# Kernel tuning notes

Hardware: AMD Instinct MI355X
Metric: run time of the kernel (lower is better)

The kernel has to match this reference:

```python
import jax, jax.numpy as jnp
import numpy as np

B, R, S, D, K = 4096, 49, 50, 512, 100

def setup_inputs() -> dict:
    key = jax.random.key(0)
    ks = jax.random.split(key, 10)
    return {
        "ifeature": jax.random.normal(ks[0], (B, R, D), dtype=jnp.float32),
        "tfeature_h": jax.random.normal(ks[1], (B, S, D), dtype=jnp.float32),
        "w_Vi_0": jax.random.normal(ks[2], (D, K), dtype=jnp.float32) * 0.05,
        "w_Vt_0": jax.random.normal(ks[3], (D, K), dtype=jnp.float32) * 0.05,
        "w_Pi_0": jax.random.normal(ks[4], (2 * K, 1), dtype=jnp.float32) * 0.05,
        "b_Pi_0": jnp.zeros((R,), dtype=jnp.float32),
        "w_Vi_1": jax.random.normal(ks[5], (D, K), dtype=jnp.float32) * 0.05,
        "w_Vt_1": jax.random.normal(ks[6], (D, K), dtype=jnp.float32) * 0.05,
        "w_Pi_1": jax.random.normal(ks[7], (2 * K, 1), dtype=jnp.float32) * 0.05,
        "b_Pi_1": jnp.zeros((S,), dtype=jnp.float32),
    }

def reference(ifeature, tfeature_h, w_Vi_0, w_Vt_0, w_Pi_0, b_Pi_0,
              w_Vi_1, w_Vt_1, w_Pi_1, b_Pi_1):
    # ---- pass 0: attend over image regions, conditioned on mean text feature
    tfeature = jnp.mean(tfeature_h, axis=1)                      # [B, D]
    wVi0 = jnp.einsum('brd,dk->brk', ifeature, w_Vi_0)           # [B, R, K]
    wVt0 = (tfeature @ w_Vt_0)[:, None, :]                       # [B, 1, K] -> broadcast over R
    Hi = jnp.tanh(jnp.concatenate(
        [wVi0, jnp.broadcast_to(wVt0, wVi0.shape)], axis=-1))    # [B, R, 2K]
    scores_i = jnp.squeeze(Hi @ w_Pi_0, axis=-1) + b_Pi_0        # [B, R]
    Pi = jax.nn.softmax(scores_i, axis=-1)                       # [B, R]
    Vi = jnp.einsum('br,brd->bd', Pi, ifeature)                  # [B, D]
    # ---- pass 1: attend over text positions, conditioned on attended image
    wVi1 = (Vi @ w_Vi_1)[:, None, :]                             # [B, 1, K]
    wVt1 = jnp.einsum('bsd,dk->bsk', tfeature_h, w_Vt_1)         # [B, S, K]
    Ht = jnp.tanh(jnp.concatenate(
        [jnp.broadcast_to(wVi1, wVt1.shape), wVt1], axis=-1))    # [B, S, 2K]
    scores_t = jnp.squeeze(Ht @ w_Pi_1, axis=-1) + b_Pi_1        # [B, S]
    Pt = jax.nn.softmax(scores_t, axis=-1)                       # [B, S]
    Vt = jnp.einsum('bs,bsd->bd', Pt, tfeature_h)                # [B, D]
    return Vi + Vt
```

## Files before the change

### kernel.cpp

```cpp
#include <hip/hip_runtime.h>
#include <math.h>

#define NB 4096
#define NR 49
#define NS 50
#define ND 512
#define NK 100
#define NTT 8
#define KSTEPS 16
#define CHUNK_KS 8
#define FRAGS (NTT * KSTEPS * 64 * 8)

typedef __attribute__((ext_vector_type(8))) short short8;
typedef __attribute__((ext_vector_type(4))) float f32x4;

__device__ __forceinline__ unsigned short f32_bf16(float f) {
    union { float f; unsigned u; } x; x.f = f;
    return (unsigned short)((x.u + 0x7fffu + ((x.u >> 16) & 1u)) >> 16);
}
__device__ __forceinline__ unsigned cvt_pk_bf16(float lo, float hi) {
    unsigned r;
    asm("v_cvt_pk_bf16_f32 %0, %1, %2" : "=v"(r) : "v"(lo), "v"(hi));
    return r;
}
__device__ __forceinline__ float fast_tanh(float x) {
    const float ax = fabsf(x);
    const float e = __expf(2.f * ax);
    const float r = 1.f - 2.f / (e + 1.f);
    return copysignf(r, x);
}

__global__ void preswz_kernel(const float* __restrict__ w0, const float* __restrict__ w1,
                              unsigned short* __restrict__ ws)
{
    const int l  = threadIdx.x;
    const int gk = blockIdx.x & 15;
    const int t  = blockIdx.x >> 4;
    const int m  = blockIdx.y;
    const float* W = m ? w1 : w0;
    const int col = t * 16 + (l & 15);
    const int k0  = gk * 32 + (l >> 4) * 8;
    unsigned short* o = ws + (size_t)m * FRAGS + ((size_t)(t * 16 + gk) * 64 + l) * 8;
#pragma unroll
    for (int j = 0; j < 8; ++j) {
        float v = (col < NK) ? W[(size_t)(k0 + j) * NK + col] : 0.f;
        o[j] = f32_bf16(v);
    }
}

struct SM {
    short buf[NS * 256];
    float scores[64];
    float part2[64];
    float P[64];
};

__global__ __launch_bounds__(512, 8) void coattn_main(
    const float* __restrict__ ifeat, const float* __restrict__ tfeat,
    const float* __restrict__ wPi0, const float* __restrict__ bPi0,
    const float* __restrict__ wPi1, const float* __restrict__ bPi1,
    const unsigned short* __restrict__ wsW, float* __restrict__ out)
{
    __shared__ SM sm;
    const int pass = blockIdx.x & 1;
    const int b    = blockIdx.x >> 1;
    const int tid  = threadIdx.x;

    const float* feat = pass ? (tfeat + (size_t)b * NS * ND) : (ifeat + (size_t)b * NR * ND);
    const int nrows  = pass ? NS : NR;
    const int nclamp = nrows - 1;
    const unsigned short* wsR = wsW + (size_t)pass * FRAGS;
    const float* wPiRow = pass ? (wPi1 + NK) : wPi0;
    const float* bvec   = pass ? bPi1 : bPi0;

    const int lane = tid & 63, wid = tid >> 6;
    const int m = wid & 3, nh = wid >> 2;
    const int t0 = nh * 4;
    const int colg = lane & 15, g = lane >> 4;
    const int arow0 = m * 16 + colg;
    const int arow = (arow0 < nclamp) ? arow0 : nclamp;
    const int rswz = arow & 7;

    const unsigned short* wlane = wsR + (size_t)t0 * (KSTEPS * 512) + lane * 8;

    const f32x4 zero4 = {0.f, 0.f, 0.f, 0.f};
    f32x4 acc[4] = {zero4, zero4, zero4, zero4};

    const int nitems = nrows * 32;

    for (int chunk = 0; chunk < 2; ++chunk) {
        __syncthreads();
        for (int it = tid; it < nitems; it += 512) {
            const int r = it >> 5, c = it & 31;
            const float* p = feat + (r << 9) + (chunk << 8) + (c << 3);
            const float4 a  = *reinterpret_cast<const float4*>(p);
            const float4 b4 = *reinterpret_cast<const float4*>(p + 4);
            uint4 v;
            v.x = cvt_pk_bf16(a.x, a.y);   v.y = cvt_pk_bf16(a.z, a.w);
            v.z = cvt_pk_bf16(b4.x, b4.y); v.w = cvt_pk_bf16(b4.z, b4.w);
            *reinterpret_cast<uint4*>(&sm.buf[(r << 8) + ((c ^ (r & 7)) << 3)]) = v;
        }
        __syncthreads();

        const int gk0 = chunk * CHUNK_KS;
#pragma unroll
        for (int ks = 0; ks < CHUNK_KS; ++ks) {
            const short8 a = *reinterpret_cast<const short8*>(
                &sm.buf[(arow << 8) + ((((ks << 2) + g) ^ rswz) << 3)]);
            const unsigned short* wk = wlane + (size_t)(gk0 + ks) * 512;
#pragma unroll
            for (int q = 0; q < 4; ++q) {
                const short8 w = *reinterpret_cast<const short8*>(wk + (size_t)q * (KSTEPS * 512));
                acc[q] = __builtin_amdgcn_mfma_f32_16x16x32_bf16(a, w, acc[q], 0, 0, 0);
            }
        }
    }

    {
        float s[4] = {0.f, 0.f, 0.f, 0.f};
#pragma unroll
        for (int q = 0; q < 4; ++q) {
            const int col = (t0 + q) * 16 + colg;
            const float w = (col < NK) ? wPiRow[col] : 0.f;
#pragma unroll
            for (int i = 0; i < 4; ++i) s[i] += fast_tanh(acc[q][i]) * w;
        }
#pragma unroll
        for (int off = 1; off < 16; off <<= 1) {
#pragma unroll
            for (int i = 0; i < 4; ++i) s[i] += __shfl_xor(s[i], off);
        }
        if (colg == 0) {
            float* o = nh ? sm.part2 : sm.scores;
            const int rbase = m * 16 + g * 4;
#pragma unroll
            for (int i = 0; i < 4; ++i) {
                const int r = rbase + i;
                if (r < nrows) o[r] = s[i] + (nh ? 0.f : bvec[r]);
            }
        }
    }
    __syncthreads();

    if (tid < 64) {
        const float v = (tid < nrows) ? sm.scores[tid] + sm.part2[tid] : -3.0e38f;
        float mx = v;
#pragma unroll
        for (int off = 32; off; off >>= 1) mx = fmaxf(mx, __shfl_xor(mx, off));
        const float e = (tid < nrows) ? __expf(v - mx) : 0.f;
        float su = e;
#pragma unroll
        for (int off = 32; off; off >>= 1) su += __shfl_xor(su, off);
        sm.P[tid] = e / su;
    }
    __syncthreads();

    {
        float v = 0.f;
        const float* fp = feat + tid;
        for (int r = 0; r < nrows; ++r) v += sm.P[r] * fp[r << 9];
        atomicAdd(&out[(size_t)b * ND + tid], v);
    }
}

extern "C" void kernel_launch(void* const* d_in, const int* in_sizes, int n_in,
                              void* d_out, int out_size, void* d_ws, size_t ws_size,
                              hipStream_t stream) {
    const float* ifeat = (const float*)d_in[0];
    const float* tfeat = (const float*)d_in[1];
    const float* wVi0  = (const float*)d_in[2];
    const float* wPi0  = (const float*)d_in[4];
    const float* bPi0  = (const float*)d_in[5];
    const float* wVt1  = (const float*)d_in[7];
    const float* wPi1  = (const float*)d_in[8];
    const float* bPi1  = (const float*)d_in[9];
    float* outp = (float*)d_out;
    unsigned short* wsW = (unsigned short*)d_ws;

    hipMemsetAsync(outp, 0, (size_t)NB * ND * sizeof(float), stream);
    hipLaunchKernelGGL(preswz_kernel, dim3(NTT * KSTEPS, 2), dim3(64), 0, stream,
                       wVi0, wVt1, wsW);
    hipLaunchKernelGGL(coattn_main, dim3(2 * NB), dim3(512), 0, stream,
                       ifeat, tfeat, wPi0, bPi0, wPi1, bPi1, wsW, outp);
}
```

Before: 338.9 us.

## Process 16 batches per block with register-resident weights and double-buffered LDS

Each block now handles 16 consecutive batch items for one pass, with 7 waves that each keep their bf16 weight column tile in registers for the whole block lifetime. Feature rows are streamed in 128-wide K chunks into double-buffered LDS, and the next chunk's global loads are issued before the current chunk's MFMAs, which overlaps loads with compute. The aim is to stop re-reading weights from global memory for every batch item and to hide load latency. In exchange the grid is much smaller (512 blocks), the kernel uses more registers, and a barrier follows every chunk.

```diff
diff --git a/kernel.cpp b/kernel.cpp
--- a/kernel.cpp
+++ b/kernel.cpp
@@ -6,10 +6,12 @@
 #define NS 50
 #define ND 512
 #define NK 100
-#define NTT 8
+#define NT 7
 #define KSTEPS 16
-#define CHUNK_KS 8
-#define FRAGS (NTT * KSTEPS * 64 * 8)
+#define NBATCH 16
+#define NGRP (NB / NBATCH)
+#define BTHREADS 448
+#define FRAGS (NT * KSTEPS * 64 * 8)
 
 typedef __attribute__((ext_vector_type(8))) short short8;
 typedef __attribute__((ext_vector_type(4))) float f32x4;
@@ -49,13 +51,12 @@
 }
 
 struct SM {
-    short buf[NS * 256];
-    float scores[64];
-    float part2[64];
+    short buf[2][64 * 128];
+    float part[NT][64];
     float P[64];
 };
 
-__global__ __launch_bounds__(512, 8) void coattn_main(
+__global__ __launch_bounds__(BTHREADS, 4) void coattn_main(
     const float* __restrict__ ifeat, const float* __restrict__ tfeat,
     const float* __restrict__ wPi0, const float* __restrict__ bPi0,
     const float* __restrict__ wPi1, const float* __restrict__ bPi1,
@@ -63,103 +64,142 @@
 {
     __shared__ SM sm;
     const int pass = blockIdx.x & 1;
-    const int b    = blockIdx.x >> 1;
+    const int grp  = blockIdx.x >> 1;
     const int tid  = threadIdx.x;
-
-    const float* feat = pass ? (tfeat + (size_t)b * NS * ND) : (ifeat + (size_t)b * NR * ND);
+    const int lane = tid & 63, wid = tid >> 6;
+    const int colg = lane & 15, g = lane >> 4;
+
     const int nrows  = pass ? NS : NR;
-    const int nclamp = nrows - 1;
-    const unsigned short* wsR = wsW + (size_t)pass * FRAGS;
+    const int nitems = nrows * 32;
+    const float* featB = (pass ? tfeat : ifeat) + (size_t)grp * NBATCH * nrows * ND;
     const float* wPiRow = pass ? (wPi1 + NK) : wPi0;
     const float* bvec   = pass ? bPi1 : bPi0;
 
-    const int lane = tid & 63, wid = tid >> 6;
-    const int m = wid & 3, nh = wid >> 2;
-    const int t0 = nh * 4;
-    const int colg = lane & 15, g = lane >> 4;
-    const int arow0 = m * 16 + colg;
-    const int arow = (arow0 < nclamp) ? arow0 : nclamp;
-    const int rswz = arow & 7;
-
-    const unsigned short* wlane = wsR + (size_t)t0 * (KSTEPS * 512) + lane * 8;
-
-    const f32x4 zero4 = {0.f, 0.f, 0.f, 0.f};
-    f32x4 acc[4] = {zero4, zero4, zero4, zero4};
-
-    const int nitems = nrows * 32;
-
-    for (int chunk = 0; chunk < 2; ++chunk) {
+    short8 wreg[KSTEPS];
+    {
+        const unsigned short* wl = wsW + (size_t)pass * FRAGS
+                                 + ((size_t)wid * KSTEPS * 64 + lane) * 8;
+#pragma unroll
+        for (int ks = 0; ks < KSTEPS; ++ks)
+            wreg[ks] = *reinterpret_cast<const short8*>(wl + ks * 512);
+    }
+
+    for (int u = tid; u < 512; u += BTHREADS) {
+        const int bsel = u >> 8, uu = u & 255;
+        const int r = 48 + (uu >> 4), q = uu & 15;
+        *reinterpret_cast<uint4*>(&sm.buf[bsel][r * 128 + q * 8]) = uint4{0u, 0u, 0u, 0u};
+    }
+    __syncthreads();
+
+    for (int it = tid; it < nitems; it += BTHREADS) {
+        const int r = it >> 5, v = it & 31;
+        const float4 a = *reinterpret_cast<const float4*>(featB + (size_t)r * ND + v * 4);
+        uint2 wv; wv.x = cvt_pk_bf16(a.x, a.y); wv.y = cvt_pk_bf16(a.z, a.w);
+        *reinterpret_cast<uint2*>(
+            &sm.buf[0][r * 128 + (((v >> 1) ^ (r & 7)) << 3) + (v & 1) * 4]) = wv;
+    }
+    __syncthreads();
+
+    const int tailN = nitems - 3 * BTHREADS;
+
+    for (int i = 0; i < NBATCH; ++i) {
+        const float* fi = featB + (size_t)i * nrows * ND;
+        f32x4 acc[4];
+#pragma unroll
+        for (int rt = 0; rt < 4; ++rt) acc[rt] = f32x4{0.f, 0.f, 0.f, 0.f};
+
+#pragma unroll
+        for (int c = 0; c < 4; ++c) {
+            const bool haveNext = (c < 3) || (i + 1 < NBATCH);
+            const float* fsrc = (c < 3) ? (fi + (c + 1) * 128) : (fi + (size_t)nrows * ND);
+
+            float4 L0{}, L1{}, L2{}, L3{};
+            if (haveNext) {
+                const int i0 = tid, i1 = tid + BTHREADS, i2 = tid + 2 * BTHREADS,
+                          i3 = tid + 3 * BTHREADS;
+                L0 = *reinterpret_cast<const float4*>(fsrc + (size_t)(i0 >> 5) * ND + (i0 & 31) * 4);
+                L1 = *reinterpret_cast<const float4*>(fsrc + (size_t)(i1 >> 5) * ND + (i1 & 31) * 4);
+                L2 = *reinterpret_cast<const float4*>(fsrc + (size_t)(i2 >> 5) * ND + (i2 & 31) * 4);
+                if (tid < tailN)
+                    L3 = *reinterpret_cast<const float4*>(fsrc + (size_t)(i3 >> 5) * ND + (i3 & 31) * 4);
+            }
+
+#pragma unroll
+            for (int lks = 0; lks < 4; ++lks) {
+                const int q0 = lks * 4 + g;
+#pragma unroll
+                for (int rt = 0; rt < 4; ++rt) {
+                    const int r = rt * 16 + colg;
+                    const short8 f = *reinterpret_cast<const short8*>(
+                        &sm.buf[c & 1][r * 128 + ((q0 ^ (r & 7)) << 3)]);
+                    acc[rt] = __builtin_amdgcn_mfma_f32_16x16x32_bf16(
+                        wreg[c * 4 + lks], f, acc[rt], 0, 0, 0);
+                }
+            }
+
+            if (haveNext) {
+                short* dst = sm.buf[(c + 1) & 1];
+                const int i0 = tid, i1 = tid + BTHREADS, i2 = tid + 2 * BTHREADS,
+                          i3 = tid + 3 * BTHREADS;
+#define WR(L, IT) { const int r = (IT) >> 5, v = (IT) & 31; \
+                    uint2 wv; wv.x = cvt_pk_bf16((L).x, (L).y); wv.y = cvt_pk_bf16((L).z, (L).w); \
+                    *reinterpret_cast<uint2*>(&dst[r * 128 + (((v >> 1) ^ (r & 7)) << 3) + (v & 1) * 4]) = wv; }
+                WR(L0, i0) WR(L1, i1) WR(L2, i2)
+                if (tid < tailN) WR(L3, i3)
+#undef WR
+            }
+            __syncthreads();
+        }
+
+        {
+            float sp[4] = {0.f, 0.f, 0.f, 0.f};
+#pragma unroll
+            for (int rt = 0; rt < 4; ++rt) {
+#pragma unroll
+                for (int ii = 0; ii < 4; ++ii) {
+                    const int n = wid * 16 + g * 4 + ii;
+                    const float w = (n < NK) ? wPiRow[n] : 0.f;
+                    sp[rt] += fast_tanh(acc[rt][ii]) * w;
+                }
+            }
+#pragma unroll
+            for (int rt = 0; rt < 4; ++rt) {
+                sp[rt] += __shfl_xor(sp[rt], 16);
+                sp[rt] += __shfl_xor(sp[rt], 32);
+            }
+            if (g == 0) {
+#pragma unroll
+                for (int rt = 0; rt < 4; ++rt)
+                    sm.part[wid][rt * 16 + colg] = sp[rt];
+            }
+        }
         __syncthreads();
-        for (int it = tid; it < nitems; it += 512) {
-            const int r = it >> 5, c = it & 31;
-            const float* p = feat + (r << 9) + (chunk << 8) + (c << 3);
-            const float4 a  = *reinterpret_cast<const float4*>(p);
-            const float4 b4 = *reinterpret_cast<const float4*>(p + 4);
-            uint4 v;
-            v.x = cvt_pk_bf16(a.x, a.y);   v.y = cvt_pk_bf16(a.z, a.w);
-            v.z = cvt_pk_bf16(b4.x, b4.y); v.w = cvt_pk_bf16(b4.z, b4.w);
-            *reinterpret_cast<uint4*>(&sm.buf[(r << 8) + ((c ^ (r & 7)) << 3)]) = v;
+
+        if (tid < 64) {
+            float v = (tid < nrows) ? bvec[tid] : 0.f;
+#pragma unroll
+            for (int w = 0; w < NT; ++w) v += sm.part[w][tid];
+            v = (tid < nrows) ? v : -3.0e38f;
+            float mx = v;
+#pragma unroll
+            for (int off = 32; off; off >>= 1) mx = fmaxf(mx, __shfl_xor(mx, off));
+            const float e = (tid < nrows) ? __expf(v - mx) : 0.f;
+            float su = e;
+#pragma unroll
+            for (int off = 32; off; off >>= 1) su += __shfl_xor(su, off);
+            sm.P[tid] = e / su;
         }
         __syncthreads();
 
-        const int gk0 = chunk * CHUNK_KS;
-#pragma unroll
-        for (int ks = 0; ks < CHUNK_KS; ++ks) {
-            const short8 a = *reinterpret_cast<const short8*>(
-                &sm.buf[(arow << 8) + ((((ks << 2) + g) ^ rswz) << 3)]);
-            const unsigned short* wk = wlane + (size_t)(gk0 + ks) * 512;
-#pragma unroll
-            for (int q = 0; q < 4; ++q) {
-                const short8 w = *reinterpret_cast<const short8*>(wk + (size_t)q * (KSTEPS * 512));
-                acc[q] = __builtin_amdgcn_mfma_f32_16x16x32_bf16(a, w, acc[q], 0, 0, 0);
-            }
-        }
-    }
-
-    {
-        float s[4] = {0.f, 0.f, 0.f, 0.f};
-#pragma unroll
-        for (int q = 0; q < 4; ++q) {
-            const int col = (t0 + q) * 16 + colg;
-            const float w = (col < NK) ? wPiRow[col] : 0.f;
-#pragma unroll
-            for (int i = 0; i < 4; ++i) s[i] += fast_tanh(acc[q][i]) * w;
-        }
-#pragma unroll
-        for (int off = 1; off < 16; off <<= 1) {
-#pragma unroll
-            for (int i = 0; i < 4; ++i) s[i] += __shfl_xor(s[i], off);
-        }
-        if (colg == 0) {
-            float* o = nh ? sm.part2 : sm.scores;
-            const int rbase = m * 16 + g * 4;
-#pragma unroll
-            for (int i = 0; i < 4; ++i) {
-                const int r = rbase + i;
-                if (r < nrows) o[r] = s[i] + (nh ? 0.f : bvec[r]);
-            }
-        }
-    }
-    __syncthreads();
-
-    if (tid < 64) {
-        const float v = (tid < nrows) ? sm.scores[tid] + sm.part2[tid] : -3.0e38f;
-        float mx = v;
-#pragma unroll
-        for (int off = 32; off; off >>= 1) mx = fmaxf(mx, __shfl_xor(mx, off));
-        const float e = (tid < nrows) ? __expf(v - mx) : 0.f;
-        float su = e;
-#pragma unroll
-        for (int off = 32; off; off >>= 1) su += __shfl_xor(su, off);
-        sm.P[tid] = e / su;
-    }
-    __syncthreads();
-
-    {
-        float v = 0.f;
-        const float* fp = feat + tid;
-        for (int r = 0; r < nrows; ++r) v += sm.P[r] * fp[r << 9];
-        atomicAdd(&out[(size_t)b * ND + tid], v);
+        {
+            const size_t bout = (size_t)(grp * NBATCH + i) * ND;
+            for (int cc = tid; cc < ND; cc += BTHREADS) {
+                float v = 0.f;
+                const float* fp = fi + cc;
+                for (int r = 0; r < nrows; ++r) v += sm.P[r] * fp[(size_t)r * ND];
+                atomicAdd(&out[bout + cc], v);
+            }
+        }
     }
 }
 
@@ -178,8 +218,8 @@
     unsigned short* wsW = (unsigned short*)d_ws;
 
     hipMemsetAsync(outp, 0, (size_t)NB * ND * sizeof(float), stream);
-    hipLaunchKernelGGL(preswz_kernel, dim3(NTT * KSTEPS, 2), dim3(64), 0, stream,
+    hipLaunchKernelGGL(preswz_kernel, dim3(NT * KSTEPS, 2), dim3(64), 0, stream,
                        wVi0, wVt1, wsW);
-    hipLaunchKernelGGL(coattn_main, dim3(2 * NB), dim3(512), 0, stream,
+    hipLaunchKernelGGL(coattn_main, dim3(2 * NGRP), dim3(BTHREADS), 0, stream,
                        ifeat, tfeat, wPi0, bPi0, wPi1, bPi1, wsW, outp);
 }
```

Measured after the change: 826.9 us. 144% more time.
